# Kernel optimization log

Hardware: AMD Instinct MI355X
Metric: run time of the kernel (lower is better)

The kernel has to match this reference:

```python
import jax, jax.numpy as jnp
import numpy as np

B, T1, T2, V, D, H = 1024, 256, 256, 32004, 50, 64


def _lstm_scan(x, h0, c0, Wih, Whh, b):
    """PyTorch-gate-order LSTM over time. x: [B,T,D]; returns hs, cs: [B,T,H]."""
    def step(carry, xt):
        h, c = carry
        g = xt @ Wih.T + h @ Whh.T + b  # [B, 4H], gate order i,f,g,o
        i, f, gg, o = jnp.split(g, 4, axis=-1)
        c = jax.nn.sigmoid(f) * c + jax.nn.sigmoid(i) * jnp.tanh(gg)
        h = jax.nn.sigmoid(o) * jnp.tanh(c)
        return (h, c), (h, c)
    _, (hs, cs) = jax.lax.scan(step, (h0, c0), jnp.swapaxes(x, 0, 1))
    return jnp.swapaxes(hs, 0, 1), jnp.swapaxes(cs, 0, 1)


def setup_inputs() -> dict:
    key = jax.random.key(0)
    ks = jax.random.split(key, 20)
    s = 1.0 / np.sqrt(H).astype(np.float32)
    inp = {
        "sentence1": jax.random.randint(ks[0], (B, T1), 0, V),
        "sentence2": jax.random.randint(ks[1], (B, T2), 0, V),
        "s1_len": jax.random.randint(ks[2], (B, 1, H), 0, T1),
        "s2_len": jax.random.randint(ks[3], (B, 1, H), 0, T2),
        "s1_s": jax.random.randint(ks[4], (B,), 0, 2),
        "s2_s": jax.random.randint(ks[5], (B,), 0, 2),
        "emb": jax.random.normal(ks[6], (V, D), jnp.float32),
        "Wih1": jax.random.uniform(ks[7], (4 * H, D), jnp.float32, -s, s),
        "Whh1": jax.random.uniform(ks[8], (4 * H, H), jnp.float32, -s, s),
        "bih1": jax.random.uniform(ks[9], (4 * H,), jnp.float32, -s, s),
        "bhh1": jax.random.uniform(ks[10], (4 * H,), jnp.float32, -s, s),
        "Wih2": jax.random.uniform(ks[11], (4 * H, D), jnp.float32, -s, s),
        "Whh2": jax.random.uniform(ks[12], (4 * H, H), jnp.float32, -s, s),
        "bih2": jax.random.uniform(ks[13], (4 * H,), jnp.float32, -s, s),
        "bhh2": jax.random.uniform(ks[14], (4 * H,), jnp.float32, -s, s),
        "Wl1": jax.random.uniform(ks[15], (128, H), jnp.float32, -s, s),
        "bl1": jax.random.uniform(ks[16], (128,), jnp.float32, -s, s),
        "Wl2": jax.random.uniform(ks[17], (4, 128), jnp.float32, -0.1, 0.1),
        "bl2": jax.random.uniform(ks[18], (4,), jnp.float32, -0.1, 0.1),
    }
    return inp


def reference(sentence1, sentence2, s1_len, s2_len, s1_s, s2_s, emb,
              Wih1, Whh1, bih1, bhh1, Wih2, Whh2, bih2, bhh2, Wl1, bl1, Wl2, bl2):
    embed1 = emb[sentence1]  # [B,T1,D]
    embed2 = emb[sentence2]  # [B,T2,D]
    h0 = jnp.zeros((B, H), embed1.dtype)
    c0 = jnp.zeros((B, H), embed1.dtype)
    # manual LSTMCell loop in original == scanned LSTM, keep all h,c per step
    h, c = _lstm_scan(embed1, h0, c0, Wih1, Whh1, bih1 + bhh1)  # [B,T1,H]
    gather_h = jnp.take_along_axis(h, s1_len, axis=1)[:, 0, :]  # [B,H]
    gather_c = jnp.take_along_axis(c, s1_len, axis=1)[:, 0, :]
    out, _ = _lstm_scan(embed2, gather_h, gather_c, Wih2, Whh2, bih2 + bhh2)
    out = jnp.take_along_axis(out, s2_len, axis=1)[:, 0, :]  # [B,H]
    out = jnp.tanh(out @ Wl1.T + bl1)  # dropout is identity at inference
    out = out @ Wl2.T + bl2  # [B,4]
    return out
```

## Files before the change

### kernel.cpp

```cpp
#include <hip/hip_runtime.h>

#define Bsz 1024
#define Tt  256
#define Vv  32004
#define Dd  50
#define Hh  64
#define MB  128

typedef __bf16 b16x8 __attribute__((ext_vector_type(8)));
typedef float  f32x4 __attribute__((ext_vector_type(4)));

__device__ __forceinline__ void barrier_novm() {
    asm volatile("s_waitcnt lgkmcnt(0)\n\ts_barrier" ::: "memory");
}
__device__ __forceinline__ float fexp2(float x) {
    float r;
    asm("v_exp_f32 %0, %1" : "=v"(r) : "v"(x));
    return r;
}
__device__ __forceinline__ float frcp(float x) {
    float r;
    asm("v_rcp_f32 %0, %1" : "=v"(r) : "v"(x));
    return r;
}
__device__ __forceinline__ float fsig_p(float x)  { return frcp(1.0f + fexp2(x)); }
__device__ __forceinline__ float ftanh_p(float x) { return 2.0f * frcp(1.0f + fexp2(x)) - 1.0f; }
__device__ __forceinline__ float ftanh(float x) {
    return 2.0f * frcp(1.0f + fexp2(x * -2.885390082f)) - 1.0f;
}

__device__ __forceinline__ void cvt_hilo(const float* x, b16x8& hi, b16x8& lo) {
#pragma unroll
    for (int e = 0; e < 8; ++e) {
        const __bf16 h = (__bf16)x[e];
        hi[e] = h;
        lo[e] = (__bf16)(x[e] - (float)h);
    }
}

__launch_bounds__(256)
__global__ void build_tables(const float* __restrict__ emb,
                             const float* __restrict__ Wih1,
                             const float* __restrict__ bih1,
                             const float* __restrict__ bhh1,
                             const float* __restrict__ Wih2,
                             const float* __restrict__ bih2,
                             const float* __restrict__ bhh2,
                             float* __restrict__ tab1,
                             float* __restrict__ tab2) {
    const int tid  = threadIdx.x;
    const int w    = tid >> 6;
    const int lane = tid & 63;
    const int q    = lane >> 4;
    const int mn   = lane & 15;
    const int v0   = blockIdx.x * MB;

    const float* Wih = blockIdx.y ? Wih2 : Wih1;
    const float* bih = blockIdx.y ? bih2 : bih1;
    const float* bhh = blockIdx.y ? bhh2 : bhh1;
    float*       tab = blockIdx.y ? tab2 : tab1;

    __shared__ __align__(16) float wlds[256 * Dd];
    __shared__ __align__(16) float elds[MB * Dd];

    for (int d4 = tid; d4 < 256 * Dd / 4; d4 += 256)
        *(float4*)&wlds[4 * d4] = *(const float4*)(Wih + 4 * d4);
    {
        const int ebase = v0 * Dd;
        const int elim  = Vv * Dd - ebase;
        const int mx    = Vv * Dd - 1;
        for (int d4 = tid; d4 < MB * Dd / 4; d4 += 256) {
            const int d = 4 * d4;
            float4 v;
            if (d + 4 <= elim) {
                v = *(const float4*)(emb + ebase + d);
            } else {
                v.x = emb[min(ebase + d,     mx)];
                v.y = emb[min(ebase + d + 1, mx)];
                v.z = emb[min(ebase + d + 2, mx)];
                v.w = emb[min(ebase + d + 3, mx)];
            }
            *(float4*)&elds[d] = v;
        }
    }
    __syncthreads();

    b16x8 bh[4][2], bl[4][2];
    f32x4 bias4;
#pragma unroll
    for (int k = 0; k < 4; ++k) {
        const int g = 64 * k + 16 * w + mn;
        const int base = g * Dd;
        float x[8];
#pragma unroll
        for (int j = 0; j < 8; ++j) x[j] = wlds[base + 8 * q + j];
        cvt_hilo(x, bh[k][0], bl[k][0]);
#pragma unroll
        for (int j = 0; j < 8; ++j) {
            const int col = 32 + 8 * q + j;
            x[j] = (col < Dd) ? wlds[base + col] : 0.0f;
        }
        cvt_hilo(x, bh[k][1], bl[k][1]);
        bias4[k] = bih[g] + bhh[g];
    }

    const f32x4 scale4 = {-1.442695041f, -1.442695041f, -2.885390082f, -1.442695041f};

#pragma unroll 1
    for (int m = 0; m < MB / 16; ++m) {
        const int base = (16 * m + mn) * Dd;
        b16x8 ah[2], al[2];
        float x[8];
#pragma unroll
        for (int j = 0; j < 8; ++j) x[j] = elds[base + 8 * q + j];
        cvt_hilo(x, ah[0], al[0]);
#pragma unroll
        for (int j = 0; j < 8; ++j) {
            const int col = 32 + 8 * q + j;
            x[j] = (col < Dd) ? elds[base + col] : 0.0f;
        }
        cvt_hilo(x, ah[1], al[1]);

        f32x4 acc[4];
#pragma unroll
        for (int k = 0; k < 4; ++k) {
            f32x4 a = {0.0f, 0.0f, 0.0f, 0.0f};
#pragma unroll
            for (int kh = 0; kh < 2; ++kh) {
                a = __builtin_amdgcn_mfma_f32_16x16x32_bf16(ah[kh], bh[k][kh], a, 0, 0, 0);
                a = __builtin_amdgcn_mfma_f32_16x16x32_bf16(ah[kh], bl[k][kh], a, 0, 0, 0);
                a = __builtin_amdgcn_mfma_f32_16x16x32_bf16(al[kh], bh[k][kh], a, 0, 0, 0);
            }
            acc[k] = a;
        }
#pragma unroll
        for (int r = 0; r < 4; ++r) {
            const int vr = v0 + 16 * m + 4 * q + r;
            if (vr < Vv) {
                f32x4 o;
                o[0] = (acc[0][r] + bias4[0]) * scale4[0];
                o[1] = (acc[1][r] + bias4[1]) * scale4[1];
                o[2] = (acc[2][r] + bias4[2]) * scale4[2];
                o[3] = (acc[3][r] + bias4[3]) * scale4[3];
                *(f32x4*)(tab + (size_t)vr * 256 + (16 * w + mn) * 4) = o;
            }
        }
    }
}

__launch_bounds__(256, 1)
__global__ void lstm_main(const int*   __restrict__ s1,
                          const int*   __restrict__ s2,
                          const int*   __restrict__ len1,
                          const int*   __restrict__ len2,
                          const float* __restrict__ tab1,
                          const float* __restrict__ tab2,
                          const float* __restrict__ Whh1,
                          const float* __restrict__ Whh2,
                          const float* __restrict__ Wl1,
                          const float* __restrict__ bl1,
                          const float* __restrict__ Wl2,
                          const float* __restrict__ bl2,
                          float* __restrict__ out) {
    const int tid  = threadIdx.x;
    const int w    = tid >> 6;
    const int lane = tid & 63;
    const int q    = lane >> 4;
    const int mn   = lane & 15;
    const int row  = mn & 3;
    const bool sb0 = (mn >> 2) & 1;
    const bool sb1 = (mn >> 3) & 1;
    const int u_own = 16 * w + 4 * q + (mn >> 2);
    const int b0   = blockIdx.x * 4;

    __shared__ __align__(16) __bf16 hsh[2][4][96];
    __shared__ __align__(16) int toklds[4][Tt + 8];
    __shared__ float h2s[4][64];
    __shared__ float ys[4][128];

    float c = 0.0f, selh = 0.0f, selc = 0.0f;
    const f32x4 zero4 = {0.0f, 0.0f, 0.0f, 0.0f};

    for (int phase = 0; phase < 2; ++phase) {
        const float* tab  = phase ? tab2 : tab1;
        const float* Whh  = phase ? Whh2 : Whh1;
        const int*   sent = phase ? s2 : s1;
        const int*   lenp = phase ? len2 : len1;

        for (int i = tid; i < 4 * Tt; i += 256)
            toklds[i >> 8][i & 255] = sent[(size_t)(b0 + (i >> 8)) * Tt + (i & 255)];

        b16x8 af[8];
#pragma unroll
        for (int k = 0; k < 4; ++k) {
            const int gate = 64 * k + 16 * w + mn;
            const float sck = (k == 2) ? -2.885390082f : -1.442695041f;
#pragma unroll
            for (int kh = 0; kh < 2; ++kh) {
                const float* ar = Whh + (size_t)gate * Hh + kh * 32 + q * 8;
                const float4 f0 = *(const float4*)ar;
                const float4 f1 = *(const float4*)(ar + 4);
                b16x8 a;
                a[0] = (__bf16)(f0.x * sck); a[1] = (__bf16)(f0.y * sck);
                a[2] = (__bf16)(f0.z * sck); a[3] = (__bf16)(f0.w * sck);
                a[4] = (__bf16)(f1.x * sck); a[5] = (__bf16)(f1.y * sck);
                a[6] = (__bf16)(f1.z * sck); a[7] = (__bf16)(f1.w * sck);
                af[2 * k + kh] = a;
            }
        }

        const int mi = lenp[(size_t)(b0 + row) * Hh + u_own];

        const float h0f = phase ? selh : 0.0f;
        c = phase ? selc : 0.0f;
        hsh[0][row][u_own] = (__bf16)h0f;
        selh = 0.0f; selc = 0.0f;
        __syncthreads();

        const float* tu = tab + 4 * u_own;

        int4 tk0 = *(const int4*)&toklds[row][0];
        int4 tkA = *(const int4*)&toklds[row][4];
        int4 tkB = *(const int4*)&toklds[row][8];

        f32x4 S0, S1, S2, S3, S4, S5, S6, S7;
        S0 = *(const f32x4*)(tu + (size_t)tk0.x * 256);
        S1 = *(const f32x4*)(tu + (size_t)tk0.y * 256);
        S2 = *(const f32x4*)(tu + (size_t)tk0.z * 256);
        S3 = *(const f32x4*)(tu + (size_t)tk0.w * 256);

        auto pick = [&](const f32x4& a) -> float {
            const float e01 = sb0 ? a[1] : a[0];
            const float e23 = sb0 ? a[3] : a[2];
            return sb1 ? e23 : e01;
        };

        auto step = [&](int i, f32x4& Su, f32x4& Sf, int tok, int tb) {
            Sf = *(const f32x4*)(tu + (size_t)tok * 256);

            const int rb = i & 1, wb = rb ^ 1;
            const b16x8 bf0 = *(const b16x8*)&hsh[rb][row][q * 8];
            const b16x8 bf1 = *(const b16x8*)&hsh[rb][row][32 + q * 8];

            f32x4 aG = __builtin_amdgcn_mfma_f32_16x16x32_bf16(af[4], bf0, zero4, 0, 0, 0);
            aG = __builtin_amdgcn_mfma_f32_16x16x32_bf16(af[5], bf1, aG, 0, 0, 0);
            f32x4 aI = __builtin_amdgcn_mfma_f32_16x16x32_bf16(af[0], bf0, zero4, 0, 0, 0);
            aI = __builtin_amdgcn_mfma_f32_16x16x32_bf16(af[1], bf1, aI, 0, 0, 0);
            f32x4 aF = __builtin_amdgcn_mfma_f32_16x16x32_bf16(af[2], bf0, zero4, 0, 0, 0);
            aF = __builtin_amdgcn_mfma_f32_16x16x32_bf16(af[3], bf1, aF, 0, 0, 0);
            f32x4 aO = __builtin_amdgcn_mfma_f32_16x16x32_bf16(af[6], bf0, zero4, 0, 0, 0);
            aO = __builtin_amdgcn_mfma_f32_16x16x32_bf16(af[7], bf1, aO, 0, 0, 0);

            const float gG = pick(aG) + Su[2];
            const float gI = pick(aI) + Su[0];
            const float gF = pick(aF) + Su[1];
            const float gO = pick(aO) + Su[3];

            const float gv = ftanh_p(gG);
            const float iv = fsig_p(gI);
            const float fv = fsig_p(gF);
            const float ov = fsig_p(gO);
            c = fv * c + iv * gv;
            const float hv = ov * ftanh(c);
            hsh[wb][row][u_own] = (__bf16)hv;
            if (tb + i == mi) { selh = hv; selc = c; }
            barrier_novm();
        };

        for (int tb = 0; tb < Tt; tb += 8) {
            step(0, S0, S4, tkA.x, tb);
            step(1, S1, S5, tkA.y, tb);
            const int nb1 = min(tb + 12, Tt - 4);
            const int4 tA2 = *(const int4*)&toklds[row][nb1];
            step(2, S2, S6, tkA.z, tb);
            const int nb2 = min(tb + 16, Tt - 4);
            const int4 tB2 = *(const int4*)&toklds[row][nb2];
            step(3, S3, S7, tkA.w, tb);
            step(4, S4, S0, tkB.x, tb);
            step(5, S5, S1, tkB.y, tb);
            step(6, S6, S2, tkB.z, tb);
            step(7, S7, S3, tkB.w, tb);
            tkA = tA2; tkB = tB2;
        }
    }

    h2s[row][u_own] = selh;
    __syncthreads();
#pragma unroll
    for (int p = 0; p < 2; ++p) {
        const int idx = tid + 256 * p;
        const int rr = idx >> 7, n = idx & 127;
        float a = bl1[n];
        const float* wl = Wl1 + n * 64;
#pragma unroll 8
        for (int k = 0; k < 64; ++k) a += h2s[rr][k] * wl[k];
        ys[rr][n] = ftanh(a);
    }
    __syncthreads();
    if (tid < 16) {
        const int rr = tid >> 2, o = tid & 3;
        float a = bl2[o];
        const float* wl = Wl2 + o * 128;
#pragma unroll 8
        for (int k = 0; k < 128; ++k) a += ys[rr][k] * wl[k];
        out[(size_t)(b0 + rr) * 4 + o] = a;
    }
}

extern "C" void kernel_launch(void* const* d_in, const int* in_sizes, int n_in,
                              void* d_out, int out_size, void* d_ws, size_t ws_size,
                              hipStream_t stream) {
    const int*   s1   = (const int*)d_in[0];
    const int*   s2   = (const int*)d_in[1];
    const int*   l1   = (const int*)d_in[2];
    const int*   l2   = (const int*)d_in[3];
    const float* emb  = (const float*)d_in[6];
    const float* Wih1 = (const float*)d_in[7];
    const float* Whh1 = (const float*)d_in[8];
    const float* bih1 = (const float*)d_in[9];
    const float* bhh1 = (const float*)d_in[10];
    const float* Wih2 = (const float*)d_in[11];
    const float* Whh2 = (const float*)d_in[12];
    const float* bih2 = (const float*)d_in[13];
    const float* bhh2 = (const float*)d_in[14];
    const float* Wl1  = (const float*)d_in[15];
    const float* bl1  = (const float*)d_in[16];
    const float* Wl2  = (const float*)d_in[17];
    const float* bl2  = (const float*)d_in[18];
    float* out = (float*)d_out;

    float* tab1 = (float*)d_ws;
    float* tab2 = tab1 + (size_t)Vv * 256;

    dim3 grid((Vv + MB - 1) / MB, 2);
    build_tables<<<grid, 256, 0, stream>>>(emb, Wih1, bih1, bhh1,
                                           Wih2, bih2, bhh2, tab1, tab2);
    lstm_main<<<Bsz / 4, 256, 0, stream>>>(s1, s2, l1, l2, tab1, tab2,
                                           Whh1, Whh2, Wl1, bl1, Wl2, bl2, out);
}
```

Baseline: 258.0 us.

## Store input projections in MFMA accumulator layout and seed MFMA with them

The precomputed embedding-projection table is now written gate-major so each lane can load its full 4-row accumulator slice per gate. Those slices are passed as the MFMA initial accumulator, so the per-step scalar gate additions go away. The prefetch depth drops from four steps to two, now with four 16-byte loads per step instead of one, and the selection check moves after the barrier. This trades more global loads per step and shorter prefetch distance for fewer VALU ops on the serial critical path; the table writes become scalar stores.

```diff
diff --git a/kernel.cpp b/kernel.cpp
--- a/kernel.cpp
+++ b/kernel.cpp
@@ -134,15 +134,13 @@
             acc[k] = a;
         }
 #pragma unroll
-        for (int r = 0; r < 4; ++r) {
-            const int vr = v0 + 16 * m + 4 * q + r;
-            if (vr < Vv) {
-                f32x4 o;
-                o[0] = (acc[0][r] + bias4[0]) * scale4[0];
-                o[1] = (acc[1][r] + bias4[1]) * scale4[1];
-                o[2] = (acc[2][r] + bias4[2]) * scale4[2];
-                o[3] = (acc[3][r] + bias4[3]) * scale4[3];
-                *(f32x4*)(tab + (size_t)vr * 256 + (16 * w + mn) * 4) = o;
+        for (int k = 0; k < 4; ++k) {
+#pragma unroll
+            for (int r = 0; r < 4; ++r) {
+                const int vr = v0 + 16 * m + 4 * q + r;
+                if (vr < Vv)
+                    tab[(size_t)vr * 256 + k * 64 + 16 * w + mn] =
+                        (acc[k][r] + bias4[k]) * scale4[k];
             }
         }
     }
@@ -179,7 +177,6 @@
     __shared__ float ys[4][128];
 
     float c = 0.0f, selh = 0.0f, selc = 0.0f;
-    const f32x4 zero4 = {0.0f, 0.0f, 0.0f, 0.0f};
 
     for (int phase = 0; phase < 2; ++phase) {
         const float* tab  = phase ? tab2 : tab1;
@@ -217,17 +214,22 @@
         selh = 0.0f; selc = 0.0f;
         __syncthreads();
 
-        const float* tu = tab + 4 * u_own;
-
-        int4 tk0 = *(const int4*)&toklds[row][0];
-        int4 tkA = *(const int4*)&toklds[row][4];
-        int4 tkB = *(const int4*)&toklds[row][8];
-
-        f32x4 S0, S1, S2, S3, S4, S5, S6, S7;
-        S0 = *(const f32x4*)(tu + (size_t)tk0.x * 256);
-        S1 = *(const f32x4*)(tu + (size_t)tk0.y * 256);
-        S2 = *(const f32x4*)(tu + (size_t)tk0.z * 256);
-        S3 = *(const f32x4*)(tu + (size_t)tk0.w * 256);
+        const float* tu = tab + 16 * w + 4 * q;
+
+        int4 C0 = *(const int4*)&toklds[row][0];
+        int4 C1 = *(const int4*)&toklds[row][4];
+        int4 C2 = *(const int4*)&toklds[row][8];
+
+        f32x4 SL0[4], SL1[4], SL2[4], SL3[4];
+        auto fill = [&](f32x4 (&S)[4], int tok) {
+            const float* tp = tu + (size_t)tok * 256;
+            S[0] = *(const f32x4*)(tp);
+            S[1] = *(const f32x4*)(tp + 64);
+            S[2] = *(const f32x4*)(tp + 128);
+            S[3] = *(const f32x4*)(tp + 192);
+        };
+        fill(SL0, C0.x);
+        fill(SL1, C0.y);
 
         auto pick = [&](const f32x4& a) -> float {
             const float e01 = sb0 ? a[1] : a[0];
@@ -235,52 +237,47 @@
             return sb1 ? e23 : e01;
         };
 
-        auto step = [&](int i, f32x4& Su, f32x4& Sf, int tok, int tb) {
-            Sf = *(const f32x4*)(tu + (size_t)tok * 256);
+        auto step = [&](int i, f32x4 (&Su)[4], f32x4 (&Sf)[4], int tok, int tb) {
+            fill(Sf, tok);
 
             const int rb = i & 1, wb = rb ^ 1;
             const b16x8 bf0 = *(const b16x8*)&hsh[rb][row][q * 8];
             const b16x8 bf1 = *(const b16x8*)&hsh[rb][row][32 + q * 8];
 
-            f32x4 aG = __builtin_amdgcn_mfma_f32_16x16x32_bf16(af[4], bf0, zero4, 0, 0, 0);
+            f32x4 aG = __builtin_amdgcn_mfma_f32_16x16x32_bf16(af[4], bf0, Su[2], 0, 0, 0);
             aG = __builtin_amdgcn_mfma_f32_16x16x32_bf16(af[5], bf1, aG, 0, 0, 0);
-            f32x4 aI = __builtin_amdgcn_mfma_f32_16x16x32_bf16(af[0], bf0, zero4, 0, 0, 0);
+            f32x4 aI = __builtin_amdgcn_mfma_f32_16x16x32_bf16(af[0], bf0, Su[0], 0, 0, 0);
             aI = __builtin_amdgcn_mfma_f32_16x16x32_bf16(af[1], bf1, aI, 0, 0, 0);
-            f32x4 aF = __builtin_amdgcn_mfma_f32_16x16x32_bf16(af[2], bf0, zero4, 0, 0, 0);
+            f32x4 aF = __builtin_amdgcn_mfma_f32_16x16x32_bf16(af[2], bf0, Su[1], 0, 0, 0);
             aF = __builtin_amdgcn_mfma_f32_16x16x32_bf16(af[3], bf1, aF, 0, 0, 0);
-            f32x4 aO = __builtin_amdgcn_mfma_f32_16x16x32_bf16(af[6], bf0, zero4, 0, 0, 0);
+            f32x4 aO = __builtin_amdgcn_mfma_f32_16x16x32_bf16(af[6], bf0, Su[3], 0, 0, 0);
             aO = __builtin_amdgcn_mfma_f32_16x16x32_bf16(af[7], bf1, aO, 0, 0, 0);
 
-            const float gG = pick(aG) + Su[2];
-            const float gI = pick(aI) + Su[0];
-            const float gF = pick(aF) + Su[1];
-            const float gO = pick(aO) + Su[3];
-
-            const float gv = ftanh_p(gG);
-            const float iv = fsig_p(gI);
-            const float fv = fsig_p(gF);
-            const float ov = fsig_p(gO);
+            const float gv = ftanh_p(pick(aG));
+            const float iv = fsig_p(pick(aI));
+            const float fv = fsig_p(pick(aF));
+            const float ov = fsig_p(pick(aO));
             c = fv * c + iv * gv;
             const float hv = ov * ftanh(c);
             hsh[wb][row][u_own] = (__bf16)hv;
+            barrier_novm();
             if (tb + i == mi) { selh = hv; selc = c; }
-            barrier_novm();
         };
 
         for (int tb = 0; tb < Tt; tb += 8) {
-            step(0, S0, S4, tkA.x, tb);
-            step(1, S1, S5, tkA.y, tb);
+            step(0, SL0, SL2, C0.z, tb);
+            step(1, SL1, SL3, C0.w, tb);
             const int nb1 = min(tb + 12, Tt - 4);
-            const int4 tA2 = *(const int4*)&toklds[row][nb1];
-            step(2, S2, S6, tkA.z, tb);
+            const int4 N1 = *(const int4*)&toklds[row][nb1];
+            step(2, SL2, SL0, C1.x, tb);
             const int nb2 = min(tb + 16, Tt - 4);
-            const int4 tB2 = *(const int4*)&toklds[row][nb2];
-            step(3, S3, S7, tkA.w, tb);
-            step(4, S4, S0, tkB.x, tb);
-            step(5, S5, S1, tkB.y, tb);
-            step(6, S6, S2, tkB.z, tb);
-            step(7, S7, S3, tkB.w, tb);
-            tkA = tA2; tkB = tB2;
+            const int4 N2 = *(const int4*)&toklds[row][nb2];
+            step(3, SL3, SL1, C1.y, tb);
+            step(4, SL0, SL2, C1.z, tb);
+            step(5, SL1, SL3, C1.w, tb);
+            step(6, SL2, SL0, C2.x, tb);
+            step(7, SL3, SL1, C2.y, tb);
+            C0 = C2; C1 = N1; C2 = N2;
         }
     }
 
```

Result: slower. 351.4 us (+36.2%).
